# Kernel tuning notes

Measured on AMD Instinct MI355X. Metric: run time of the kernel, lower is better.

Reference implementation:

```python
import jax, jax.numpy as jnp
import numpy as np

KERNEL_MUL = 2.0
KERNEL_NUM = 5


def setup_inputs() -> dict:
    key = jax.random.key(0)
    k1, k2 = jax.random.split(key)
    source = jax.random.normal(k1, (4096, 256), dtype=jnp.float32)
    target = jax.random.normal(k2, (4096, 256), dtype=jnp.float32)
    return {"source": source, "target": target}


def _mmd(source, target):
    b = source.shape[0]
    total = jnp.concatenate([source, target], axis=0)  # [2N, D]
    n = total.shape[0]
    # pairwise squared L2 via gram trick (avoids O(N^2 * D) intermediate)
    sq = jnp.sum(total * total, axis=1)  # [2N]
    d2 = sq[:, None] + sq[None, :] - 2.0 * (total @ total.T)
    d2 = jnp.maximum(d2, 0.0)  # [2N, 2N]
    # bandwidth from detached distances (matches L2_distance.data)
    bandwidth = jax.lax.stop_gradient(jnp.sum(d2)) / (n * n - n)
    bandwidth = bandwidth / (KERNEL_MUL ** (KERNEL_NUM // 2))
    kernels = jnp.zeros_like(d2)
    for i in range(KERNEL_NUM):
        kernels = kernels + jnp.exp(-d2 / (bandwidth * KERNEL_MUL ** i))
    XX = kernels[:b, :b]
    YY = kernels[b:, b:]
    XY = kernels[:b, b:]
    YX = kernels[b:, :b]
    return jnp.mean(XX + YY - XY - YX)


def reference(source, target):
    return _mmd(source, target)
```

## Files before the change

### kernel.cpp

```cpp
#include <hip/hip_runtime.h>
#include <hip/hip_bf16.h>


#define N_TOTAL 8192
#define B_HALF 4096
#define D_DIM 256
#define NTILE 64
#define NPAIR 1056

typedef float f32x16 __attribute__((ext_vector_type(16)));
typedef _Float16 f16x8 __attribute__((ext_vector_type(8)));

__device__ __forceinline__ const float* row_base(const float* src, const float* tgt, int r) {
    return (r < B_HALF) ? src + (size_t)r * D_DIM : tgt + (size_t)(r - B_HALF) * D_DIM;
}

__global__ __launch_bounds__(256) void prep_kernel(const float* __restrict__ src,
                                                   const float* __restrict__ tgt,
                                                   _Float16* __restrict__ a16f,
                                                   float* __restrict__ sq,
                                                   float* __restrict__ colpart,
                                                   unsigned* __restrict__ cnt) {
    int tid = threadIdx.x, w = tid >> 6, lane = tid & 63;
    int r0 = blockIdx.x * 32;
    if (blockIdx.x == 0 && tid == 0) *cnt = 0;

    #pragma unroll
    for (int i = 0; i < 8; ++i) {
        int row = r0 + w * 8 + i;
        const float* rp = row_base(src, tgt, row);
        float4 v = ((const float4*)rp)[lane];
        float s = v.x*v.x + v.y*v.y + v.z*v.z + v.w*v.w;
        #pragma unroll
        for (int off = 32; off; off >>= 1) s += __shfl_down(s, off, 64);
        if (lane == 0) sq[row] = s;
    }

    float c = 0.f;
    for (int r = r0; r < r0 + 32; ++r)
        c += row_base(src, tgt, r)[tid];
    colpart[blockIdx.x * D_DIM + tid] = c;

    int wg = blockIdx.x * 4 + w;
    #pragma unroll
    for (int i = 0; i < 4; ++i) {
        int t  = wg * 4 + i;
        int kb = t >> 7, rg = t & 127;
        int row = rg * 64 + lane;
        const float* rp = row_base(src, tgt, row) + kb * 8;
        float4 v0 = ((const float4*)rp)[0];
        float4 v1 = ((const float4*)rp)[1];
        _Float16 h[8] = {(_Float16)v0.x, (_Float16)v0.y, (_Float16)v0.z, (_Float16)v0.w,
                         (_Float16)v1.x, (_Float16)v1.y, (_Float16)v1.z, (_Float16)v1.w};
        *(f16x8*)(a16f + ((size_t)kb * N_TOTAL + row) * 8) = *(f16x8*)h;
    }
}

__global__ __launch_bounds__(256) void bw_kernel(const float* __restrict__ sq,
                                                 const float* __restrict__ colpart,
                                                 float* __restrict__ negc,
                                                 double* __restrict__ accum) {
    __shared__ double red[256];
    int t = threadIdx.x;
    double s = 0.0;
    for (int i = t; i < N_TOTAL; i += 256) s += (double)sq[i];
    red[t] = s;
    __syncthreads();
    for (int off = 128; off; off >>= 1) {
        if (t < off) red[t] += red[t + off];
        __syncthreads();
    }
    double sumsq = red[0];
    __syncthreads();
    float c = 0.f;
    for (int k = 0; k < 256; ++k) c += colpart[k * D_DIM + t];
    red[t] = (double)c * (double)c;
    __syncthreads();
    for (int off = 128; off; off >>= 1) {
        if (t < off) red[t] += red[t + off];
        __syncthreads();
    }
    if (t == 0) {
        double S1 = 2.0 * (double)N_TOTAL * sumsq - 2.0 * red[0];
        double nn = (double)N_TOTAL * (double)N_TOTAL - (double)N_TOTAL;
        double bw = S1 / nn / 4.0;
        negc[0] = (float)(-1.4426950408889634 / (16.0 * bw));
        accum[0] = 0.0;
    }
}

__global__ __launch_bounds__(512) void mmd_main(const _Float16* __restrict__ a16f,
                                                const float* __restrict__ sq,
                                                const float* __restrict__ negc,
                                                double* __restrict__ accum,
                                                unsigned* __restrict__ cnt,
                                                float* __restrict__ out) {
    __shared__ float wsum[8];

    int b  = blockIdx.x;
    int bs = (b & 7) * (NPAIR / 8) + (b >> 3);
    int it = 0, cum = 0;
    while (cum + (32 - (it >> 1)) <= bs) { cum += 32 - (it >> 1); ++it; }
    int p = (it >> 1) + (bs - cum);

    int tid = threadIdx.x, lane = tid & 63, wid = tid >> 6;
    int wrow = wid >> 2, wcol = wid & 3;
    int jt   = 2 * p + (wcol >> 1);
    int rowA = it * 128 + wrow * 64;
    int rowB = jt * 128 + (wcol & 1) * 64;
    int c32 = lane & 31, khalf = lane >> 5;

    const _Float16* PA = a16f + (size_t)khalf * (N_TOTAL * 8)
                              + (size_t)(rowA + c32) * 8;
    const _Float16* PB = a16f + (size_t)khalf * (N_TOTAL * 8)
                              + (size_t)(rowB + c32) * 8;

    f32x16 acc[2][2] = {};

    #pragma unroll 4
    for (int kap = 0; kap < 16; ++kap) {
        size_t ko = (size_t)kap * (N_TOTAL * 16);
        f16x8 af[2], bf[2];
        af[0] = *(const f16x8*)(PA + ko);
        af[1] = *(const f16x8*)(PA + ko + 32 * 8);
        bf[0] = *(const f16x8*)(PB + ko);
        bf[1] = *(const f16x8*)(PB + ko + 32 * 8);
        __builtin_amdgcn_s_setprio(1);
        #pragma unroll
        for (int mt = 0; mt < 2; ++mt)
            #pragma unroll
            for (int nt = 0; nt < 2; ++nt)
                acc[mt][nt] = __builtin_amdgcn_mfma_f32_32x32x16_f16(af[mt], bf[nt], acc[mt][nt], 0, 0, 0);
        __builtin_amdgcn_s_setprio(0);
    }

    float nc = *negc;
    float m2nc = -2.f * nc;
    float sj1[2];
    #pragma unroll
    for (int nt = 0; nt < 2; ++nt)
        sj1[nt] = nc * sq[rowB + nt * 32 + c32];
    float tu = 0.f, t2 = 0.f;
    #pragma unroll
    for (int mt = 0; mt < 2; ++mt) {
        #pragma unroll
        for (int reg = 0; reg < 16; ++reg) {
            int i = rowA + mt * 32 + (reg & 3) + 8 * (reg >> 2) + 4 * khalf;
            float si1 = nc * sq[i];
            #pragma unroll
            for (int nt = 0; nt < 2; ++nt) {
                float e  = fminf(fmaf(m2nc, acc[mt][nt][reg], si1 + sj1[nt]), 0.f);
                float u  = exp2f(e);
                float u2 = u * u, u4 = u2 * u2, u8 = u4 * u4;
                float in2 = fmaf(u4, 1.f + u8, 1.f);
                float in3 = fmaf(u2, in2, 1.f);
                tu += u;
                t2  = fmaf(u2, in3, t2);
            }
        }
    }
    float scale = 0.f;
    if (jt >= it)
        scale = (((it < 32) == (jt < 32)) ? 1.f : -1.f) * ((it == jt) ? 1.f : 2.f);
    float tsum = (tu + t2) * scale;

    #pragma unroll
    for (int off = 32; off; off >>= 1) tsum += __shfl_down(tsum, off, 64);
    if (lane == 0) wsum[wid] = tsum;
    __syncthreads();
    if (tid == 0) {
        float t = 0.f;
        #pragma unroll
        for (int w = 0; w < 8; ++w) t += wsum[w];
        atomicAdd(accum, (double)t);
        __threadfence();
        unsigned old = atomicAdd(cnt, 1u);
        if (old == NPAIR - 1) {
            double v = atomicAdd(accum, 0.0);
            out[0] = (float)(v / ((double)B_HALF * (double)B_HALF));
        }
    }
}

extern "C" void kernel_launch(void* const* d_in, const int* in_sizes, int n_in,
                              void* d_out, int out_size, void* d_ws, size_t ws_size,
                              hipStream_t stream) {
    const float* src = (const float*)d_in[0];
    const float* tgt = (const float*)d_in[1];
    float* out = (float*)d_out;

    char* ws = (char*)d_ws;
    float*    sq      = (float*)ws;
    float*    colpart = (float*)(ws + 32768);
    float*    negc    = (float*)(ws + 294912);
    double*   accum   = (double*)(ws + 294920);
    unsigned* cnt     = (unsigned*)(ws + 294928);
    _Float16* a16f    = (_Float16*)(ws + 327680);

    prep_kernel<<<256, 256, 0, stream>>>(src, tgt, a16f, sq, colpart, cnt);
    bw_kernel<<<1, 256, 0, stream>>>(sq, colpart, negc, accum);
    mmd_main<<<NPAIR, 512, 0, stream>>>(a16f, sq, negc, accum, cnt, out);
}
```

Baseline: 86.11 us.

## Map one 256-thread block per triangular tile to skip lower-triangle work

Changes the grid from blocks covering pairs of column tiles (some of which fell below the diagonal and were zero-weighted) to one 256-thread block per upper-triangular 128x128 tile. This removes the wasted MFMA and exp work on below-diagonal tiles and gives finer-grained scheduling. It also drops the s_setprio hints, raises the k-loop unroll, and sets a min-blocks-per-CU launch bound. The cost is more blocks and more atomics on the shared accumulator.

```diff
diff --git a/kernel.cpp b/kernel.cpp
--- a/kernel.cpp
+++ b/kernel.cpp
@@ -5,8 +5,9 @@
 #define N_TOTAL 8192
 #define B_HALF 4096
 #define D_DIM 256
+#define TILE 128
 #define NTILE 64
-#define NPAIR 1056
+#define NTRI 2080
 
 typedef float f32x16 __attribute__((ext_vector_type(16)));
 typedef _Float16 f16x8 __attribute__((ext_vector_type(8)));
@@ -89,35 +90,33 @@
     }
 }
 
-__global__ __launch_bounds__(512) void mmd_main(const _Float16* __restrict__ a16f,
-                                                const float* __restrict__ sq,
-                                                const float* __restrict__ negc,
-                                                double* __restrict__ accum,
-                                                unsigned* __restrict__ cnt,
-                                                float* __restrict__ out) {
-    __shared__ float wsum[8];
+__global__ __launch_bounds__(256, 4) void mmd_main(const _Float16* __restrict__ a16f,
+                                                   const float* __restrict__ sq,
+                                                   const float* __restrict__ negc,
+                                                   double* __restrict__ accum,
+                                                   unsigned* __restrict__ cnt,
+                                                   float* __restrict__ out) {
+    __shared__ float wsum[4];
 
     int b  = blockIdx.x;
-    int bs = (b & 7) * (NPAIR / 8) + (b >> 3);
+    int bs = (b & 7) * (NTRI / 8) + (b >> 3);
     int it = 0, cum = 0;
-    while (cum + (32 - (it >> 1)) <= bs) { cum += 32 - (it >> 1); ++it; }
-    int p = (it >> 1) + (bs - cum);
+    while (cum + (NTILE - it) <= bs) { cum += NTILE - it; ++it; }
+    int jt = it + (bs - cum);
 
     int tid = threadIdx.x, lane = tid & 63, wid = tid >> 6;
-    int wrow = wid >> 2, wcol = wid & 3;
-    int jt   = 2 * p + (wcol >> 1);
-    int rowA = it * 128 + wrow * 64;
-    int rowB = jt * 128 + (wcol & 1) * 64;
+    int wrow = wid >> 1, wcol = wid & 1;
+    int rowA = it * TILE, rowB = jt * TILE;
     int c32 = lane & 31, khalf = lane >> 5;
 
     const _Float16* PA = a16f + (size_t)khalf * (N_TOTAL * 8)
-                              + (size_t)(rowA + c32) * 8;
+                              + (size_t)(rowA + wrow * 64 + c32) * 8;
     const _Float16* PB = a16f + (size_t)khalf * (N_TOTAL * 8)
-                              + (size_t)(rowB + c32) * 8;
+                              + (size_t)(rowB + wcol * 64 + c32) * 8;
 
     f32x16 acc[2][2] = {};
 
-    #pragma unroll 4
+    #pragma unroll 8
     for (int kap = 0; kap < 16; ++kap) {
         size_t ko = (size_t)kap * (N_TOTAL * 16);
         f16x8 af[2], bf[2];
@@ -125,13 +124,11 @@
         af[1] = *(const f16x8*)(PA + ko + 32 * 8);
         bf[0] = *(const f16x8*)(PB + ko);
         bf[1] = *(const f16x8*)(PB + ko + 32 * 8);
-        __builtin_amdgcn_s_setprio(1);
         #pragma unroll
         for (int mt = 0; mt < 2; ++mt)
             #pragma unroll
             for (int nt = 0; nt < 2; ++nt)
                 acc[mt][nt] = __builtin_amdgcn_mfma_f32_32x32x16_f16(af[mt], bf[nt], acc[mt][nt], 0, 0, 0);
-        __builtin_amdgcn_s_setprio(0);
     }
 
     float nc = *negc;
@@ -139,13 +136,13 @@
     float sj1[2];
     #pragma unroll
     for (int nt = 0; nt < 2; ++nt)
-        sj1[nt] = nc * sq[rowB + nt * 32 + c32];
+        sj1[nt] = nc * sq[rowB + wcol * 64 + nt * 32 + c32];
     float tu = 0.f, t2 = 0.f;
     #pragma unroll
     for (int mt = 0; mt < 2; ++mt) {
         #pragma unroll
         for (int reg = 0; reg < 16; ++reg) {
-            int i = rowA + mt * 32 + (reg & 3) + 8 * (reg >> 2) + 4 * khalf;
+            int i = rowA + wrow * 64 + mt * 32 + (reg & 3) + 8 * (reg >> 2) + 4 * khalf;
             float si1 = nc * sq[i];
             #pragma unroll
             for (int nt = 0; nt < 2; ++nt) {
@@ -159,9 +156,7 @@
             }
         }
     }
-    float scale = 0.f;
-    if (jt >= it)
-        scale = (((it < 32) == (jt < 32)) ? 1.f : -1.f) * ((it == jt) ? 1.f : 2.f);
+    float scale = (((it < 32) == (jt < 32)) ? 1.f : -1.f) * ((it == jt) ? 1.f : 2.f);
     float tsum = (tu + t2) * scale;
 
     #pragma unroll
@@ -169,13 +164,11 @@
     if (lane == 0) wsum[wid] = tsum;
     __syncthreads();
     if (tid == 0) {
-        float t = 0.f;
-        #pragma unroll
-        for (int w = 0; w < 8; ++w) t += wsum[w];
+        float t = wsum[0] + wsum[1] + wsum[2] + wsum[3];
         atomicAdd(accum, (double)t);
         __threadfence();
         unsigned old = atomicAdd(cnt, 1u);
-        if (old == NPAIR - 1) {
+        if (old == NTRI - 1) {
             double v = atomicAdd(accum, 0.0);
             out[0] = (float)(v / ((double)B_HALF * (double)B_HALF));
         }
@@ -199,5 +192,5 @@
 
     prep_kernel<<<256, 256, 0, stream>>>(src, tgt, a16f, sq, colpart, cnt);
     bw_kernel<<<1, 256, 0, stream>>>(sq, colpart, negc, accum);
-    mmd_main<<<NPAIR, 512, 0, stream>>>(a16f, sq, negc, accum, cnt, out);
+    mmd_main<<<NTRI, 256, 0, stream>>>(a16f, sq, negc, accum, cnt, out);
 }
```

Result: slower. 105.7 us (+22.7%).
